# Kernel optimization log

Measured on AMD Instinct MI355X. Metric: run time of the kernel, lower is better.

Reference implementation:

```python
import jax, jax.numpy as jnp
import numpy as np

EPSILON = 0.3
ALPHA = 0.7
LN_EPS = 1e-5


def _layernorm(x, g, b):
    mu = jnp.mean(x, axis=-1, keepdims=True)
    var = jnp.mean((x - mu) ** 2, axis=-1, keepdims=True)
    return (x - mu) / jnp.sqrt(var + LN_EPS) * g + b


def setup_inputs() -> dict:
    key = jax.random.key(0)
    ks = jax.random.split(key, 6)
    B, N, D, L = 1, 2048, 768, 16
    s = 0.05  # weight scale to keep sigmoid/exp well-conditioned
    return {
        "x": jax.random.normal(ks[0], (B, N, D), jnp.float32),
        "proj_w": jax.random.normal(ks[1], (D, L), jnp.float32) * s,
        "proj_b": jnp.zeros((L,), jnp.float32),
        "ln1_g": jnp.ones((L,), jnp.float32),
        "ln1_b": jnp.zeros((L,), jnp.float32),
        "pi_w1": jax.random.normal(ks[2], (L, D), jnp.float32) * s,
        "pi_b1": jnp.zeros((D,), jnp.float32),
        "pi_w2": jax.random.normal(ks[3], (D, 1), jnp.float32) * s,
        "pi_b2": jnp.zeros((1,), jnp.float32),
        "dt": jnp.full((1,), 0.05, jnp.float32),
        "f_w": jax.random.normal(ks[4], (D, D), jnp.float32) * s,
        "f_b": jnp.zeros((D,), jnp.float32),
        "ln2_g": jnp.ones((D,), jnp.float32),
        "ln2_b": jnp.zeros((D,), jnp.float32),
    }


def reference(x, proj_w, proj_b, ln1_g, ln1_b, pi_w1, pi_b1, pi_w2, pi_b2, dt, f_w, f_b, ln2_g, ln2_b):
    B, N, D = x.shape
    # proj_list: Linear -> LayerNorm -> ReLU. [B,N,L]
    x_proj = jax.nn.relu(_layernorm(x @ proj_w + proj_b, ln1_g, ln1_b))
    # RBF kernel over pairwise differences. [B,N,N]
    diff = x_proj[:, :, None, :] - x_proj[:, None, :, :]
    K_eps = jnp.exp(-(1.0 / (4.0 * EPSILON)) * jnp.sum(diff * diff, axis=-1))
    q_tilde = jnp.sum(K_eps, axis=2)  # [B,N]
    # pi_list: Linear -> ReLU -> Linear -> Sigmoid. [B,N]
    pi = jax.nn.sigmoid(jax.nn.relu(x_proj @ pi_w1 + pi_b1) @ pi_w2 + pi_b2)[..., 0]
    v = pi / q_tilde  # diagonal of D_epsilon_tilde
    # K_tilde = K_eps @ diag(v): column scaling (math-equivalent to bmm with diag_embed)
    K_tilde = K_eps * v[:, None, :]
    d = jnp.sum(K_tilde, axis=2) + 1e-5  # diagonal of D_tilde
    # inv(D_tilde) @ K_tilde: row scaling; then subtract identity
    L_op = (1.0 / EPSILON) * (K_tilde / d[:, :, None]) - jnp.eye(N, dtype=x.dtype)[None]
    L_mat = L_op[0]  # .squeeze(0), B == 1
    # f(x): modeled as linear map
    target = x @ f_w + f_b  # [B,N,D]
    tt = dt * jnp.einsum('ij,bjd->bid', L_mat, target)  # target_transformed
    target1 = target + tt
    target2 = ALPHA * x + (1.0 - ALPHA) * (target1 + tt)
    return _layernorm(target2, ln2_g, ln2_b)
```

## Files before the change

### kernel.cpp

```cpp
#include <hip/hip_runtime.h>
#include <math.h>

#define EPSILON 0.3f
#define ALPHA 0.7f
#define LN_EPS 1e-5f

typedef __bf16 bf16x8 __attribute__((ext_vector_type(8)));
typedef float f32x4 __attribute__((ext_vector_type(4)));

__device__ __forceinline__ unsigned short f2bf(float f) {
  unsigned int u = __float_as_uint(f);
  return (unsigned short)((u + 0x7fffu + ((u >> 16) & 1u)) >> 16);
}
__device__ __forceinline__ float bf2f(unsigned short h) {
  return __uint_as_float(((unsigned int)h) << 16);
}
__device__ __forceinline__ unsigned int pack2(float lo, float hi) {
  return (unsigned int)f2bf(lo) | ((unsigned int)f2bf(hi) << 16);
}

__device__ __forceinline__ float wave_reduce(float v) {
#pragma unroll
  for (int off = 32; off > 0; off >>= 1) v += __shfl_xor(v, off, 64);
  return v;
}

__device__ __forceinline__ float blk_reduce_sum(float v, float* red) {
  v = wave_reduce(v);
  int lane = threadIdx.x & 63, wid = threadIdx.x >> 6;
  __syncthreads();
  if (lane == 0) red[wid] = v;
  __syncthreads();
  float s = 0.f;
  int nw = (blockDim.x + 63) >> 6;
  for (int w = 0; w < nw; ++w) s += red[w];
  return s;
}

__global__ __launch_bounds__(256) void k_proj(
    const float* __restrict__ x, const float* __restrict__ proj_w,
    const float* __restrict__ proj_b, const float* __restrict__ ln1_g,
    const float* __restrict__ ln1_b, const float* __restrict__ pi_w1,
    const float* __restrict__ pi_b1, const float* __restrict__ pi_w2,
    const float* __restrict__ pi_b2, float* __restrict__ xp,
    float* __restrict__ s, float* __restrict__ pi, int N, int D) {
  __shared__ float xs[16][68];
  __shared__ float ws[64][20];
  __shared__ float ysh[16][17];
  __shared__ float xps[16][16];
  __shared__ float pr[16][4];
  int tid = threadIdx.x;
  int row0 = blockIdx.x * 16;
  int row = tid >> 4, l = tid & 15;
  int lane = tid & 63, w = tid >> 6;
  int skc = (tid & 15) * 4;
  int wk = tid >> 2, wl = (tid & 3) * 4;
  float acc = 0.f;
  for (int k0 = 0; k0 < D; k0 += 64) {
    float4 xv = *(const float4*)(x + (size_t)(row0 + row) * D + k0 + skc);
    float4 wv = *(const float4*)(proj_w + (size_t)(k0 + wk) * 16 + wl);
    __syncthreads();
    *(float4*)&xs[row][skc] = xv;
    *(float4*)&ws[wk][wl] = wv;
    __syncthreads();
#pragma unroll
    for (int kk = 0; kk < 64; kk += 4) {
      float4 a4 = *(const float4*)&xs[row][kk];
      acc += a4.x * ws[kk + 0][l];
      acc += a4.y * ws[kk + 1][l];
      acc += a4.z * ws[kk + 2][l];
      acc += a4.w * ws[kk + 3][l];
    }
  }
  float y = acc + proj_b[l];
  ysh[row][l] = y;
  __syncthreads();
  float mu = 0.f;
#pragma unroll
  for (int t = 0; t < 16; ++t) mu += ysh[row][t];
  mu *= (1.f / 16.f);
  float var = 0.f;
#pragma unroll
  for (int t = 0; t < 16; ++t) { float d2 = ysh[row][t] - mu; var += d2 * d2; }
  var *= (1.f / 16.f);
  float rstd = rsqrtf(var + LN_EPS);
  float xpv = fmaxf((y - mu) * rstd * ln1_g[l] + ln1_b[l], 0.f);
  xps[row][l] = xpv;
  xp[(size_t)(row0 + row) * 16 + l] = xpv;
  float sq = xpv * xpv;
  sq += __shfl_xor(sq, 8, 64);
  sq += __shfl_xor(sq, 4, 64);
  sq += __shfl_xor(sq, 2, 64);
  sq += __shfl_xor(sq, 1, 64);
  if ((lane & 15) == 0) s[row0 + row] = sq;
  __syncthreads();
  float w1r[3][16], b1r[3], w2r[3];
#pragma unroll
  for (int c = 0; c < 3; ++c) {
    int d0 = tid + c * 256;
    b1r[c] = pi_b1[d0];
    w2r[c] = pi_w2[d0];
#pragma unroll
    for (int t = 0; t < 16; ++t) w1r[c][t] = pi_w1[(size_t)t * D + d0];
  }
  float pacc[16];
#pragma unroll
  for (int r = 0; r < 16; ++r) pacc[r] = 0.f;
#pragma unroll
  for (int r = 0; r < 16; ++r) {
    float xv[16];
#pragma unroll
    for (int t4 = 0; t4 < 4; ++t4) {
      float4 xq = *(const float4*)&xps[r][t4 * 4];
      xv[t4 * 4 + 0] = xq.x; xv[t4 * 4 + 1] = xq.y;
      xv[t4 * 4 + 2] = xq.z; xv[t4 * 4 + 3] = xq.w;
    }
    float pa = 0.f;
#pragma unroll
    for (int c = 0; c < 3; ++c) {
      float h = b1r[c];
#pragma unroll
      for (int t = 0; t < 16; ++t) h += xv[t] * w1r[c][t];
      h = fmaxf(h, 0.f);
      pa += h * w2r[c];
    }
    pacc[r] = pa;
  }
#pragma unroll
  for (int r = 0; r < 16; ++r) {
    float pv = wave_reduce(pacc[r]);
    if (lane == 0) pr[r][w] = pv;
  }
  __syncthreads();
  if (tid < 16) {
    float tot = pr[tid][0] + pr[tid][1] + pr[tid][2] + pr[tid][3] + pi_b2[0];
    pi[row0 + tid] = 1.f / (1.f + expf(-tot));
  }
}

__global__ __launch_bounds__(256) void k_keps(
    const float* __restrict__ xp, const float* __restrict__ s,
    const float* __restrict__ pi, unsigned short* __restrict__ Kb,
    float* __restrict__ q, float* __restrict__ v, int N) {
  __shared__ float qs[4][4];
  int i0 = blockIdx.x * 4;
  int tid = threadIdx.x, lane = tid & 63, w = tid >> 6;
  float a[4][16], si[4];
#pragma unroll
  for (int r = 0; r < 4; ++r) {
    const float* ap = xp + (size_t)(i0 + r) * 16;
#pragma unroll
    for (int t = 0; t < 16; ++t) a[r][t] = ap[t];
    si[r] = s[i0 + r];
  }
  const float c = 1.f / (4.f * EPSILON);
  float qa[4] = {0.f, 0.f, 0.f, 0.f};
  for (int it = 0; it < N / 256; ++it) {
    int j = it * 256 + tid;
    const float4* bp = (const float4*)(xp + (size_t)j * 16);
    float4 b0 = bp[0], b1 = bp[1], b2 = bp[2], b3 = bp[3];
    float bv[16] = {b0.x, b0.y, b0.z, b0.w, b1.x, b1.y, b1.z, b1.w,
                    b2.x, b2.y, b2.z, b2.w, b3.x, b3.y, b3.z, b3.w};
    float sj = s[j];
#pragma unroll
    for (int r = 0; r < 4; ++r) {
      float dot = 0.f;
#pragma unroll
      for (int t = 0; t < 16; ++t) dot += a[r][t] * bv[t];
      float kv = expf(-c * (si[r] + sj - 2.f * dot));
      Kb[(size_t)(i0 + r) * N + j] = f2bf(kv);
      qa[r] += kv;
    }
  }
#pragma unroll
  for (int r = 0; r < 4; ++r) {
    float t = wave_reduce(qa[r]);
    if (lane == 0) qs[r][w] = t;
  }
  __syncthreads();
  if (tid < 4) {
    float tot = qs[tid][0] + qs[tid][1] + qs[tid][2] + qs[tid][3];
    q[i0 + tid] = tot;
    v[i0 + tid] = pi[i0 + tid] / tot;
  }
}

__global__ __launch_bounds__(256) void k_scale_bf(
    const unsigned short* __restrict__ Kb, const float* __restrict__ v,
    float* __restrict__ dv, int N) {
  __shared__ float red[4];
  int i = blockIdx.x, tid = threadIdx.x;
  float acc = 0.f;
  for (int j8 = tid * 8; j8 < N; j8 += 256 * 8) {
    uint4 kv4 = *(const uint4*)(Kb + (size_t)i * N + j8);
    float4 va = *(const float4*)(v + j8);
    float4 vb = *(const float4*)(v + j8 + 4);
    unsigned int u;
    u = kv4.x;
    acc += __uint_as_float(u << 16) * va.x + __uint_as_float(u & 0xffff0000u) * va.y;
    u = kv4.y;
    acc += __uint_as_float(u << 16) * va.z + __uint_as_float(u & 0xffff0000u) * va.w;
    u = kv4.z;
    acc += __uint_as_float(u << 16) * vb.x + __uint_as_float(u & 0xffff0000u) * vb.y;
    u = kv4.w;
    acc += __uint_as_float(u << 16) * vb.z + __uint_as_float(u & 0xffff0000u) * vb.w;
  }
  float tot = blk_reduce_sum(acc, red);
  if (tid == 0) dv[i] = tot + 1e-5f;
}

__global__ __launch_bounds__(256) void k_tcvt(
    const float* __restrict__ src, unsigned short* __restrict__ dst,
    int R, int C) {
  __shared__ unsigned short tile[32][33];
  int tx = threadIdx.x & 31, ty = threadIdx.x >> 5;
  int r0 = blockIdx.y * 32, c0 = blockIdx.x * 32;
#pragma unroll
  for (int i = 0; i < 4; ++i) {
    int r = r0 + ty + i * 8;
    tile[ty + i * 8][tx] = f2bf(src[(size_t)r * C + c0 + tx]);
  }
  __syncthreads();
#pragma unroll
  for (int i = 0; i < 4; ++i) {
    int cc = c0 + ty + i * 8;
    dst[(size_t)cc * R + r0 + tx] = tile[tx][ty + i * 8];
  }
}

__global__ __launch_bounds__(256) void k_gemm1(
    const float* __restrict__ x, const unsigned short* __restrict__ Bt,
    const float* __restrict__ bias, const float* __restrict__ v,
    float* __restrict__ T, unsigned short* __restrict__ Ttb,
    int M, int N, int K) {
  __shared__ unsigned short As[64][72];
  __shared__ unsigned short Bs[64][72];
  int tid = threadIdx.x;
  int w = tid >> 6, l = tid & 63;
  int ln = l & 15, quad = l >> 4;
  int mh = (w & 1) * 32, nh = (w >> 1) * 32;
  int row0 = blockIdx.y * 64, col0 = blockIdx.x * 64;
  int lr = tid >> 3, lc = (tid & 7) * 8;
  f32x4 acc[2][2] = {};
  for (int k0 = 0; k0 < K; k0 += 64) {
    float4 a00 = *(const float4*)(x + (size_t)(row0 + lr) * K + k0 + lc);
    float4 a01 = *(const float4*)(x + (size_t)(row0 + lr) * K + k0 + lc + 4);
    float4 a10 = *(const float4*)(x + (size_t)(row0 + lr + 32) * K + k0 + lc);
    float4 a11 = *(const float4*)(x + (size_t)(row0 + lr + 32) * K + k0 + lc + 4);
    uint4 b0 = *(const uint4*)(Bt + (size_t)(col0 + lr) * K + k0 + lc);
    uint4 b1 = *(const uint4*)(Bt + (size_t)(col0 + lr + 32) * K + k0 + lc);
    __syncthreads();
    *(uint4*)&As[lr][lc] =
        make_uint4(pack2(a00.x, a00.y), pack2(a00.z, a00.w),
                   pack2(a01.x, a01.y), pack2(a01.z, a01.w));
    *(uint4*)&As[lr + 32][lc] =
        make_uint4(pack2(a10.x, a10.y), pack2(a10.z, a10.w),
                   pack2(a11.x, a11.y), pack2(a11.z, a11.w));
    *(uint4*)&Bs[lr][lc] = b0;
    *(uint4*)&Bs[lr + 32][lc] = b1;
    __syncthreads();
#pragma unroll
    for (int ks = 0; ks < 2; ++ks) {
      bf16x8 bfr[2], afr[2];
#pragma unroll
      for (int nt = 0; nt < 2; ++nt)
        bfr[nt] = *(const bf16x8*)&Bs[nh + nt * 16 + ln][ks * 32 + quad * 8];
#pragma unroll
      for (int mt = 0; mt < 2; ++mt)
        afr[mt] = *(const bf16x8*)&As[mh + mt * 16 + ln][ks * 32 + quad * 8];
#pragma unroll
      for (int mt = 0; mt < 2; ++mt)
#pragma unroll
        for (int nt = 0; nt < 2; ++nt)
          acc[mt][nt] = __builtin_amdgcn_mfma_f32_16x16x32_bf16(
              afr[mt], bfr[nt], acc[mt][nt], 0, 0, 0);
    }
  }
#pragma unroll
  for (int mt = 0; mt < 2; ++mt)
#pragma unroll
    for (int nt = 0; nt < 2; ++nt) {
      int col = col0 + nh + nt * 16 + ln;
      float bv = bias[col];
#pragma unroll
      for (int r = 0; r < 4; ++r) {
        int row = row0 + mh + mt * 16 + quad * 4 + r;
        float tv = acc[mt][nt][r] + bv;
        T[(size_t)row * N + col] = tv;
        Ttb[(size_t)col * M + row] = f2bf(v[row] * tv);
      }
    }
}

__global__ __launch_bounds__(256) void k_gemm2(
    const unsigned short* __restrict__ A, const unsigned short* __restrict__ Bt,
    const float* __restrict__ x, const float* __restrict__ T,
    const float* __restrict__ dv, const float* __restrict__ dtp,
    float* __restrict__ out, int M, int N, int K) {
  __shared__ unsigned short As[64][72];
  __shared__ unsigned short Bs[64][72];
  int tid = threadIdx.x;
  int w = tid >> 6, l = tid & 63;
  int ln = l & 15, quad = l >> 4;
  int mh = (w & 1) * 32, nh = (w >> 1) * 32;
  int row0 = blockIdx.y * 64, col0 = blockIdx.x * 64;
  int lr = tid >> 3, lc = (tid & 7) * 8;
  f32x4 acc[2][2] = {};
  for (int k0 = 0; k0 < K; k0 += 64) {
    uint4 a0 = *(const uint4*)(A + (size_t)(row0 + lr) * K + k0 + lc);
    uint4 a1 = *(const uint4*)(A + (size_t)(row0 + lr + 32) * K + k0 + lc);
    uint4 b0 = *(const uint4*)(Bt + (size_t)(col0 + lr) * K + k0 + lc);
    uint4 b1 = *(const uint4*)(Bt + (size_t)(col0 + lr + 32) * K + k0 + lc);
    __syncthreads();
    *(uint4*)&As[lr][lc] = a0;
    *(uint4*)&As[lr + 32][lc] = a1;
    *(uint4*)&Bs[lr][lc] = b0;
    *(uint4*)&Bs[lr + 32][lc] = b1;
    __syncthreads();
#pragma unroll
    for (int ks = 0; ks < 2; ++ks) {
      bf16x8 bfr[2], afr[2];
#pragma unroll
      for (int nt = 0; nt < 2; ++nt)
        bfr[nt] = *(const bf16x8*)&Bs[nh + nt * 16 + ln][ks * 32 + quad * 8];
#pragma unroll
      for (int mt = 0; mt < 2; ++mt)
        afr[mt] = *(const bf16x8*)&As[mh + mt * 16 + ln][ks * 32 + quad * 8];
#pragma unroll
      for (int mt = 0; mt < 2; ++mt)
#pragma unroll
        for (int nt = 0; nt < 2; ++nt)
          acc[mt][nt] = __builtin_amdgcn_mfma_f32_16x16x32_bf16(
              afr[mt], bfr[nt], acc[mt][nt], 0, 0, 0);
    }
  }
  float dtv = dtp[0];
  float c2 = (1.f - ALPHA) * (1.f - 2.f * dtv);
  float c3b = (1.f - ALPHA) * 2.f * dtv / EPSILON;
#pragma unroll
  for (int mt = 0; mt < 2; ++mt)
#pragma unroll
    for (int nt = 0; nt < 2; ++nt) {
      int col = col0 + nh + nt * 16 + ln;
#pragma unroll
      for (int r = 0; r < 4; ++r) {
        int row = row0 + mh + mt * 16 + quad * 4 + r;
        size_t idx = (size_t)row * N + col;
        float c3 = c3b / dv[row];
        out[idx] = ALPHA * x[idx] + c2 * T[idx] + c3 * acc[mt][nt][r];
      }
    }
}

__global__ __launch_bounds__(256) void k_ln_rows(
    float* __restrict__ out, const float* __restrict__ g,
    const float* __restrict__ b, int D) {
  __shared__ float red[4];
  int i = blockIdx.x, tid = threadIdx.x;
  float v[4];
  int nt = D / 256;
  float sum = 0.f;
  for (int t = 0; t < nt; ++t) {
    v[t] = out[(size_t)i * D + tid + t * 256];
    sum += v[t];
  }
  float mu = blk_reduce_sum(sum, red) / (float)D;
  float sq = 0.f;
  for (int t = 0; t < nt; ++t) { float d2 = v[t] - mu; sq += d2 * d2; }
  float var = blk_reduce_sum(sq, red) / (float)D;
  float rs = rsqrtf(var + LN_EPS);
  for (int t = 0; t < nt; ++t) {
    int d0 = tid + t * 256;
    out[(size_t)i * D + d0] = (v[t] - mu) * rs * g[d0] + b[d0];
  }
}

extern "C" void kernel_launch(void* const* d_in, const int* in_sizes, int n_in,
                              void* d_out, int out_size, void* d_ws, size_t ws_size,
                              hipStream_t stream) {
  const float* x = (const float*)d_in[0];
  const float* proj_w = (const float*)d_in[1];
  const float* proj_b = (const float*)d_in[2];
  const float* ln1_g = (const float*)d_in[3];
  const float* ln1_b = (const float*)d_in[4];
  const float* pi_w1 = (const float*)d_in[5];
  const float* pi_b1 = (const float*)d_in[6];
  const float* pi_w2 = (const float*)d_in[7];
  const float* pi_b2 = (const float*)d_in[8];
  const float* dt = (const float*)d_in[9];
  const float* f_w = (const float*)d_in[10];
  const float* f_b = (const float*)d_in[11];
  const float* ln2_g = (const float*)d_in[12];
  const float* ln2_b = (const float*)d_in[13];
  float* out = (float*)d_out;

  int D = in_sizes[11];
  int N = in_sizes[0] / D;

  unsigned short* Kb = (unsigned short*)d_ws;
  float* T = (float*)(Kb + (size_t)N * N);
  unsigned short* Ttb = (unsigned short*)(T + (size_t)N * D);
  unsigned short* fwTb = Ttb + (size_t)D * N;
  float* xp = (float*)(fwTb + (size_t)D * D);
  float* s = xp + (size_t)N * 16;
  float* pi = s + N;
  float* q = pi + N;
  float* v = q + N;
  float* dv = v + N;

  k_proj<<<N / 16, 256, 0, stream>>>(x, proj_w, proj_b, ln1_g, ln1_b, pi_w1,
                                     pi_b1, pi_w2, pi_b2, xp, s, pi, N, D);
  k_keps<<<N / 4, 256, 0, stream>>>(xp, s, pi, Kb, q, v, N);
  k_scale_bf<<<N, 256, 0, stream>>>(Kb, v, dv, N);
  k_tcvt<<<dim3(D / 32, D / 32), 256, 0, stream>>>(f_w, fwTb, D, D);
  k_gemm1<<<dim3(D / 64, N / 64), 256, 0, stream>>>(x, fwTb, f_b, v, T, Ttb,
                                                    N, D, D);
  k_gemm2<<<dim3(D / 64, N / 64), 256, 0, stream>>>(Kb, Ttb, x, T, dv, dt, out,
                                                    N, D, N);
  k_ln_rows<<<N, 256, 0, stream>>>(out, ln2_g, ln2_b, D);
}
```

Baseline: 167.6 us.

## Split-K both GEMMs with reduction kernels, fuse epilogue into layernorm

Both GEMMs now split the K dimension across a third grid axis (2-way for the f(x) GEMM, 4-way for the L@target GEMM), writing fp32 partials to workspace. A new reduce kernel sums the first GEMM's partials, adds the bias and writes T and the transposed, v-scaled bf16 copy through a shared-memory tile. The second GEMM's partial sum and the alpha/T/dv epilogue are fused into the final layernorm kernel. The K_eps kernel also processes two columns per thread with packed bf16 stores. The intent is to fill more CUs with the small 32x12 tile grid, at the cost of extra partial-buffer traffic and two more kernel launches.

Measured after the change: 165.3 us. No clear change (-1.4%).

```diff
diff --git a/kernel.cpp b/kernel.cpp
--- a/kernel.cpp
+++ b/kernel.cpp
@@ -155,21 +155,25 @@
   }
   const float c = 1.f / (4.f * EPSILON);
   float qa[4] = {0.f, 0.f, 0.f, 0.f};
-  for (int it = 0; it < N / 256; ++it) {
-    int j = it * 256 + tid;
+  for (int it = 0; it < N / 512; ++it) {
+    int j = it * 512 + tid * 2;
     const float4* bp = (const float4*)(xp + (size_t)j * 16);
     float4 b0 = bp[0], b1 = bp[1], b2 = bp[2], b3 = bp[3];
+    float4 c0 = bp[4], c1 = bp[5], c2 = bp[6], c3 = bp[7];
     float bv[16] = {b0.x, b0.y, b0.z, b0.w, b1.x, b1.y, b1.z, b1.w,
                     b2.x, b2.y, b2.z, b2.w, b3.x, b3.y, b3.z, b3.w};
-    float sj = s[j];
+    float cv[16] = {c0.x, c0.y, c0.z, c0.w, c1.x, c1.y, c1.z, c1.w,
+                    c2.x, c2.y, c2.z, c2.w, c3.x, c3.y, c3.z, c3.w};
+    float sj0 = s[j], sj1 = s[j + 1];
 #pragma unroll
     for (int r = 0; r < 4; ++r) {
-      float dot = 0.f;
-#pragma unroll
-      for (int t = 0; t < 16; ++t) dot += a[r][t] * bv[t];
-      float kv = expf(-c * (si[r] + sj - 2.f * dot));
-      Kb[(size_t)(i0 + r) * N + j] = f2bf(kv);
-      qa[r] += kv;
+      float d0 = 0.f, d1 = 0.f;
+#pragma unroll
+      for (int t = 0; t < 16; ++t) { d0 += a[r][t] * bv[t]; d1 += a[r][t] * cv[t]; }
+      float k0 = expf(-c * (si[r] + sj0 - 2.f * d0));
+      float k1 = expf(-c * (si[r] + sj1 - 2.f * d1));
+      *(unsigned int*)(Kb + (size_t)(i0 + r) * N + j) = pack2(k0, k1);
+      qa[r] += k0 + k1;
     }
   }
 #pragma unroll
@@ -230,9 +234,7 @@
 
 __global__ __launch_bounds__(256) void k_gemm1(
     const float* __restrict__ x, const unsigned short* __restrict__ Bt,
-    const float* __restrict__ bias, const float* __restrict__ v,
-    float* __restrict__ T, unsigned short* __restrict__ Ttb,
-    int M, int N, int K) {
+    float* __restrict__ P, int M, int N, int K, int klen) {
   __shared__ unsigned short As[64][72];
   __shared__ unsigned short Bs[64][72];
   int tid = threadIdx.x;
@@ -240,9 +242,10 @@
   int ln = l & 15, quad = l >> 4;
   int mh = (w & 1) * 32, nh = (w >> 1) * 32;
   int row0 = blockIdx.y * 64, col0 = blockIdx.x * 64;
+  int ks = blockIdx.z * klen;
   int lr = tid >> 3, lc = (tid & 7) * 8;
   f32x4 acc[2][2] = {};
-  for (int k0 = 0; k0 < K; k0 += 64) {
+  for (int k0 = ks; k0 < ks + klen; k0 += 64) {
     float4 a00 = *(const float4*)(x + (size_t)(row0 + lr) * K + k0 + lc);
     float4 a01 = *(const float4*)(x + (size_t)(row0 + lr) * K + k0 + lc + 4);
     float4 a10 = *(const float4*)(x + (size_t)(row0 + lr + 32) * K + k0 + lc);
@@ -260,14 +263,14 @@
     *(uint4*)&Bs[lr + 32][lc] = b1;
     __syncthreads();
 #pragma unroll
-    for (int ks = 0; ks < 2; ++ks) {
+    for (int kss = 0; kss < 2; ++kss) {
       bf16x8 bfr[2], afr[2];
 #pragma unroll
       for (int nt = 0; nt < 2; ++nt)
-        bfr[nt] = *(const bf16x8*)&Bs[nh + nt * 16 + ln][ks * 32 + quad * 8];
+        bfr[nt] = *(const bf16x8*)&Bs[nh + nt * 16 + ln][kss * 32 + quad * 8];
 #pragma unroll
       for (int mt = 0; mt < 2; ++mt)
-        afr[mt] = *(const bf16x8*)&As[mh + mt * 16 + ln][ks * 32 + quad * 8];
+        afr[mt] = *(const bf16x8*)&As[mh + mt * 16 + ln][kss * 32 + quad * 8];
 #pragma unroll
       for (int mt = 0; mt < 2; ++mt)
 #pragma unroll
@@ -276,27 +279,48 @@
               afr[mt], bfr[nt], acc[mt][nt], 0, 0, 0);
     }
   }
+  float* Ps = P + (size_t)blockIdx.z * M * N;
 #pragma unroll
   for (int mt = 0; mt < 2; ++mt)
 #pragma unroll
     for (int nt = 0; nt < 2; ++nt) {
       int col = col0 + nh + nt * 16 + ln;
-      float bv = bias[col];
 #pragma unroll
       for (int r = 0; r < 4; ++r) {
         int row = row0 + mh + mt * 16 + quad * 4 + r;
-        float tv = acc[mt][nt][r] + bv;
-        T[(size_t)row * N + col] = tv;
-        Ttb[(size_t)col * M + row] = f2bf(v[row] * tv);
+        Ps[(size_t)row * N + col] = acc[mt][nt][r];
       }
     }
+}
+
+__global__ __launch_bounds__(256) void k_red1(
+    const float* __restrict__ P, const float* __restrict__ bias,
+    const float* __restrict__ v, float* __restrict__ T,
+    unsigned short* __restrict__ Ttb, int M, int N) {
+  __shared__ unsigned short tile[32][33];
+  int tx = threadIdx.x & 31, ty = threadIdx.x >> 5;
+  int r0 = blockIdx.y * 32, c0 = blockIdx.x * 32;
+  const float* P1 = P + (size_t)M * N;
+  float bv = bias[c0 + tx];
+#pragma unroll
+  for (int i = 0; i < 4; ++i) {
+    int r = r0 + ty + i * 8;
+    size_t idx = (size_t)r * N + c0 + tx;
+    float tv = P[idx] + P1[idx] + bv;
+    T[idx] = tv;
+    tile[ty + i * 8][tx] = f2bf(v[r] * tv);
+  }
+  __syncthreads();
+#pragma unroll
+  for (int i = 0; i < 4; ++i) {
+    int cc = c0 + ty + i * 8;
+    Ttb[(size_t)cc * M + r0 + tx] = tile[tx][ty + i * 8];
+  }
 }
 
 __global__ __launch_bounds__(256) void k_gemm2(
     const unsigned short* __restrict__ A, const unsigned short* __restrict__ Bt,
-    const float* __restrict__ x, const float* __restrict__ T,
-    const float* __restrict__ dv, const float* __restrict__ dtp,
-    float* __restrict__ out, int M, int N, int K) {
+    float* __restrict__ Q, int M, int N, int K, int klen) {
   __shared__ unsigned short As[64][72];
   __shared__ unsigned short Bs[64][72];
   int tid = threadIdx.x;
@@ -304,9 +328,10 @@
   int ln = l & 15, quad = l >> 4;
   int mh = (w & 1) * 32, nh = (w >> 1) * 32;
   int row0 = blockIdx.y * 64, col0 = blockIdx.x * 64;
+  int ks = blockIdx.z * klen;
   int lr = tid >> 3, lc = (tid & 7) * 8;
   f32x4 acc[2][2] = {};
-  for (int k0 = 0; k0 < K; k0 += 64) {
+  for (int k0 = ks; k0 < ks + klen; k0 += 64) {
     uint4 a0 = *(const uint4*)(A + (size_t)(row0 + lr) * K + k0 + lc);
     uint4 a1 = *(const uint4*)(A + (size_t)(row0 + lr + 32) * K + k0 + lc);
     uint4 b0 = *(const uint4*)(Bt + (size_t)(col0 + lr) * K + k0 + lc);
@@ -318,14 +343,14 @@
     *(uint4*)&Bs[lr + 32][lc] = b1;
     __syncthreads();
 #pragma unroll
-    for (int ks = 0; ks < 2; ++ks) {
+    for (int kss = 0; kss < 2; ++kss) {
       bf16x8 bfr[2], afr[2];
 #pragma unroll
       for (int nt = 0; nt < 2; ++nt)
-        bfr[nt] = *(const bf16x8*)&Bs[nh + nt * 16 + ln][ks * 32 + quad * 8];
+        bfr[nt] = *(const bf16x8*)&Bs[nh + nt * 16 + ln][kss * 32 + quad * 8];
 #pragma unroll
       for (int mt = 0; mt < 2; ++mt)
-        afr[mt] = *(const bf16x8*)&As[mh + mt * 16 + ln][ks * 32 + quad * 8];
+        afr[mt] = *(const bf16x8*)&As[mh + mt * 16 + ln][kss * 32 + quad * 8];
 #pragma unroll
       for (int mt = 0; mt < 2; ++mt)
 #pragma unroll
@@ -334,44 +359,48 @@
               afr[mt], bfr[nt], acc[mt][nt], 0, 0, 0);
     }
   }
+  float* Qs = Q + (size_t)blockIdx.z * M * N;
+#pragma unroll
+  for (int mt = 0; mt < 2; ++mt)
+#pragma unroll
+    for (int nt = 0; nt < 2; ++nt) {
+      int col = col0 + nh + nt * 16 + ln;
+#pragma unroll
+      for (int r = 0; r < 4; ++r) {
+        int row = row0 + mh + mt * 16 + quad * 4 + r;
+        Qs[(size_t)row * N + col] = acc[mt][nt][r];
+      }
+    }
+}
+
+__global__ __launch_bounds__(256) void k_red2_ln(
+    const float* __restrict__ Q, const float* __restrict__ x,
+    const float* __restrict__ T, const float* __restrict__ dv,
+    const float* __restrict__ dtp, const float* __restrict__ g,
+    const float* __restrict__ b, float* __restrict__ out, int D, size_t MN) {
+  __shared__ float red[4];
+  int i = blockIdx.x, tid = threadIdx.x;
   float dtv = dtp[0];
   float c2 = (1.f - ALPHA) * (1.f - 2.f * dtv);
-  float c3b = (1.f - ALPHA) * 2.f * dtv / EPSILON;
-#pragma unroll
-  for (int mt = 0; mt < 2; ++mt)
-#pragma unroll
-    for (int nt = 0; nt < 2; ++nt) {
-      int col = col0 + nh + nt * 16 + ln;
-#pragma unroll
-      for (int r = 0; r < 4; ++r) {
-        int row = row0 + mh + mt * 16 + quad * 4 + r;
-        size_t idx = (size_t)row * N + col;
-        float c3 = c3b / dv[row];
-        out[idx] = ALPHA * x[idx] + c2 * T[idx] + c3 * acc[mt][nt][r];
-      }
-    }
-}
-
-__global__ __launch_bounds__(256) void k_ln_rows(
-    float* __restrict__ out, const float* __restrict__ g,
-    const float* __restrict__ b, int D) {
-  __shared__ float red[4];
-  int i = blockIdx.x, tid = threadIdx.x;
-  float v[4];
+  float c3 = (1.f - ALPHA) * 2.f * dtv / EPSILON / dv[i];
+  float vv[4];
   int nt = D / 256;
   float sum = 0.f;
   for (int t = 0; t < nt; ++t) {
-    v[t] = out[(size_t)i * D + tid + t * 256];
-    sum += v[t];
+    size_t idx = (size_t)i * D + tid + t * 256;
+    float acc = Q[idx] + Q[idx + MN] + Q[idx + 2 * MN] + Q[idx + 3 * MN];
+    float val = ALPHA * x[idx] + c2 * T[idx] + c3 * acc;
+    vv[t] = val;
+    sum += val;
   }
   float mu = blk_reduce_sum(sum, red) / (float)D;
   float sq = 0.f;
-  for (int t = 0; t < nt; ++t) { float d2 = v[t] - mu; sq += d2 * d2; }
+  for (int t = 0; t < nt; ++t) { float d2 = vv[t] - mu; sq += d2 * d2; }
   float var = blk_reduce_sum(sq, red) / (float)D;
   float rs = rsqrtf(var + LN_EPS);
   for (int t = 0; t < nt; ++t) {
     int d0 = tid + t * 256;
-    out[(size_t)i * D + d0] = (v[t] - mu) * rs * g[d0] + b[d0];
+    out[(size_t)i * D + d0] = (vv[t] - mu) * rs * g[d0] + b[d0];
   }
 }
 
@@ -401,7 +430,9 @@
   float* T = (float*)(Kb + (size_t)N * N);
   unsigned short* Ttb = (unsigned short*)(T + (size_t)N * D);
   unsigned short* fwTb = Ttb + (size_t)D * N;
-  float* xp = (float*)(fwTb + (size_t)D * D);
+  float* P = (float*)(fwTb + (size_t)D * D);
+  float* Q = P + (size_t)2 * N * D;
+  float* xp = Q + (size_t)4 * N * D;
   float* s = xp + (size_t)N * 16;
   float* pi = s + N;
   float* q = pi + N;
@@ -413,9 +444,11 @@
   k_keps<<<N / 4, 256, 0, stream>>>(xp, s, pi, Kb, q, v, N);
   k_scale_bf<<<N, 256, 0, stream>>>(Kb, v, dv, N);
   k_tcvt<<<dim3(D / 32, D / 32), 256, 0, stream>>>(f_w, fwTb, D, D);
-  k_gemm1<<<dim3(D / 64, N / 64), 256, 0, stream>>>(x, fwTb, f_b, v, T, Ttb,
-                                                    N, D, D);
-  k_gemm2<<<dim3(D / 64, N / 64), 256, 0, stream>>>(Kb, Ttb, x, T, dv, dt, out,
-                                                    N, D, N);
-  k_ln_rows<<<N, 256, 0, stream>>>(out, ln2_g, ln2_b, D);
-}
+  k_gemm1<<<dim3(D / 64, N / 64, 2), 256, 0, stream>>>(x, fwTb, P, N, D, D,
+                                                       D / 2);
+  k_red1<<<dim3(D / 32, N / 32), 256, 0, stream>>>(P, f_b, v, T, Ttb, N, D);
+  k_gemm2<<<dim3(D / 64, N / 64, 4), 256, 0, stream>>>(Kb, Ttb, Q, N, D, N,
+                                                       N / 4);
+  k_red2_ln<<<N, 256, 0, stream>>>(Q, x, T, dv, dt, ln2_g, ln2_b, out, D,
+                                   (size_t)N * D);
+}
```
